# Kernel tuning notes

Hardware: AMD Instinct MI355X
Metric: run time of the kernel (lower is better)

Reference implementation:

```python
import jax, jax.numpy as jnp
import numpy as np

STRIDE = 1
PAD = 1

def setup_inputs() -> dict:
    key = jax.random.key(0)
    k1, k2 = jax.random.split(key)
    x = jax.random.normal(k1, (32, 128, 56, 56), dtype=jnp.float32)
    weight = jax.random.normal(k2, (256, 128, 3, 3), dtype=jnp.float32) * 0.1
    b = jnp.zeros((256,), dtype=jnp.float32)
    return {"x": x, "weight": weight, "b": b}

def reference(x, weight, b):
    # Binarize weights with sign (matches torch.sign: sign(0)=0), then plain conv2d.
    bw = jnp.sign(weight)
    out = jax.lax.conv_general_dilated(
        x, bw,
        window_strides=(STRIDE, STRIDE),
        padding=((PAD, PAD), (PAD, PAD)),
        dimension_numbers=("NCHW", "OIHW", "NCHW"),
    )
    return out + b[None, :, None, None]
```

## Files before the change

### kernel.cpp

```cpp
#include <hip/hip_runtime.h>
#include <hip/hip_bf16.h>

typedef __attribute__((ext_vector_type(8))) short bf16x8;
typedef __attribute__((ext_vector_type(4))) float f32x4;

#define CIN   128
#define COUT  256
#define NIMG  32
#define HWDIM 56
#define HPAD  58
#define KTOT  1152
#define HWIMG 3136
#define MTOT  100352
#define BN    256
#define BK    64
#define NT    18
#define BSZA  (COUT * BK)

__device__ __forceinline__ void gload16(const void* g, void* l) {
  __builtin_amdgcn_global_load_lds((const __attribute__((address_space(1))) void*)g,
                                   (__attribute__((address_space(3))) void*)l,
                                   16, 0, 0);
}

__global__ __launch_bounds__(256)
void prep_all(const float* __restrict__ x, const float* __restrict__ w,
              __hip_bfloat16* __restrict__ xp, __hip_bfloat16* __restrict__ wt) {
  __shared__ float tile[CIN * 57];
  const int bid = blockIdx.x;
  const int t = threadIdx.x;
  if (bid < NIMG * HPAD) {
    const int n = bid / HPAD;
    const int h = bid - n * HPAD;
    __hip_bfloat16* dstrow = xp + ((size_t)n * HPAD + h) * HPAD * CIN;
    int4 z; z.x = 0; z.y = 0; z.z = 0; z.w = 0;
    if (h == 0 || h == HPAD - 1) {
      for (int i = t; i < (HPAD * CIN) / 8; i += 256)
        reinterpret_cast<int4*>(dstrow)[i] = z;
      return;
    }
    const float* src = x + (size_t)n * CIN * HWIMG + (size_t)(h - 1) * HWDIM;
    for (int i = t; i < CIN * HWDIM; i += 256) {
      int c = i / HWDIM;
      int wd = i - c * HWDIM;
      tile[c * 57 + wd] = src[(size_t)c * HWIMG + wd];
    }
    if (t < 32) {
      int side = t >> 4;
      reinterpret_cast<int4*>(dstrow + (side ? (HPAD - 1) : 0) * CIN)[t & 15] = z;
    }
    __syncthreads();
    __hip_bfloat16* dst = dstrow + CIN;
    for (int o = t; o < HWDIM * 64; o += 256) {
      int wd = o >> 6;
      int c = (o & 63) * 2;
      __hip_bfloat162 pr;
      pr.x = __float2bfloat16(tile[c * 57 + wd]);
      pr.y = __float2bfloat16(tile[(c + 1) * 57 + wd]);
      *reinterpret_cast<__hip_bfloat162*>(dst + (size_t)wd * CIN + c) = pr;
    }
  } else {
    int o = (bid - NIMG * HPAD) * 256 + t;
    int cout = o / KTOT;
    int r = o - cout * KTOT;
    int tap = r >> 7;
    int cin = r & 127;
    float v = w[((size_t)cout * CIN + cin) * 9 + tap];
    wt[o] = __float2bfloat16(v > 0.f ? 1.f : (v < 0.f ? -1.f : 0.f));
  }
}

__global__ __launch_bounds__(512, 2)
void bconv(const short* __restrict__ xp, const short* __restrict__ wt,
           const float* __restrict__ bias, float* __restrict__ out) {
  __shared__ short lds[2][2 * BSZA];

  const int tid  = threadIdx.x;
  const int lane = tid & 63;
  const int wv   = tid >> 6;
  const int wm   = wv >> 2;
  const int wn   = wv & 3;
  const int s0   = blockIdx.x * BN;

  const int srow = tid >> 3;
  const int swz  = (tid & 7) ^ (srow & 7);

  int xb[2][2];
#pragma unroll
  for (int h = 0; h < 2; ++h)
#pragma unroll
    for (int r = 0; r < 2; ++r) {
      int m  = s0 + h * 128 + r * 64 + srow;
      int n  = m / HWIMG;
      int hw = m - n * HWIMG;
      int hh = hw / HWDIM;
      int ww = hw - hh * HWDIM;
      xb[h][r] = ((n * HPAD + hh) * HPAD + ww) * CIN + swz * 8;
    }
  const int wb = srow * KTOT + swz * 8;

#define STAGE_A(C, H, R, KO) \
  gload16(wt + ((H) * 128 + (R) * 64) * KTOT + wb + (KO), \
          &lds[C][(((H) * 128 + (R) * 64) + wv * 8) * BK])
#define STAGE_B(C, H, R, XKO) \
  gload16(xp + xb[H][R] + (XKO), \
          &lds[C][BSZA + (((H) * 128 + (R) * 64) + wv * 8) * BK])

  const int rlo = lane & 15;
  const int kq  = lane >> 4;
  const int swr = rlo & 7;

  f32x4 acc[8][4] = {};
  bf16x8 bx[4][2], af[2][2];

#define AF_LOAD(Q) \
  _Pragma("unroll") for (int f = 0; f < 2; ++f) \
  _Pragma("unroll") for (int kk = 0; kk < 2; ++kk) \
    af[f][kk] = *(const bf16x8*)&A[((Q) * 64 + wm * 32 + f * 16 + rlo) * BK + ((kk * 4 + kq) ^ swr) * 8];

#define MFMA_CLUSTER(Q) \
  __builtin_amdgcn_s_barrier(); \
  asm volatile("s_waitcnt lgkmcnt(0)" ::: "memory"); \
  __builtin_amdgcn_sched_barrier(0); \
  __builtin_amdgcn_s_setprio(1); \
  _Pragma("unroll") for (int f = 0; f < 2; ++f) \
  _Pragma("unroll") for (int nf = 0; nf < 4; ++nf) \
  _Pragma("unroll") for (int kk = 0; kk < 2; ++kk) \
    acc[2 * (Q) + f][nf] = __builtin_amdgcn_mfma_f32_16x16x32_bf16(af[f][kk], bx[nf][kk], acc[2 * (Q) + f][nf], 0, 0, 0); \
  __builtin_amdgcn_s_setprio(0);

  STAGE_B(0, 0, 0, 0); STAGE_B(0, 0, 1, 0);
  STAGE_B(0, 1, 0, 0); STAGE_B(0, 1, 1, 0);
  STAGE_A(0, 0, 0, 0); STAGE_A(0, 0, 1, 0);
  STAGE_A(0, 1, 0, 0); STAGE_A(0, 1, 1, 0);
  asm volatile("s_waitcnt vmcnt(0)" ::: "memory");
  __builtin_amdgcn_s_barrier();

  for (int t = 0; t < NT; ++t) {
    const int c  = t & 1;
    const int cn = c ^ 1;
    const short* A = &lds[c][0];
    const short* B = &lds[c][BSZA];
    const bool st = (t + 1 < NT);
    const int t1   = t + 1;
    const int tap1 = t1 >> 1;
    const int kh1  = tap1 / 3;
    const int kw1  = tap1 - kh1 * 3;
    const int xko1 = (kh1 * HPAD + kw1) * CIN + (t1 & 1) * BK;
    const int ko1  = t1 * BK;

#pragma unroll
    for (int nf = 0; nf < 4; ++nf)
#pragma unroll
      for (int kk = 0; kk < 2; ++kk)
        bx[nf][kk] = *(const bf16x8*)&B[(wn * 64 + nf * 16 + rlo) * BK + ((kk * 4 + kq) ^ swr) * 8];
    AF_LOAD(0)
    if (st) { STAGE_B(cn, 0, 0, xko1); STAGE_B(cn, 0, 1, xko1); }
    MFMA_CLUSTER(0)
    __builtin_amdgcn_s_barrier();

    AF_LOAD(1)
    if (st) { STAGE_B(cn, 1, 0, xko1); STAGE_B(cn, 1, 1, xko1); }
    MFMA_CLUSTER(1)
    if (st) asm volatile("s_waitcnt vmcnt(4)" ::: "memory");
    else    asm volatile("s_waitcnt vmcnt(0)" ::: "memory");
    __builtin_amdgcn_s_barrier();

    AF_LOAD(2)
    if (st) { STAGE_A(cn, 0, 0, ko1); STAGE_A(cn, 0, 1, ko1); }
    MFMA_CLUSTER(2)
    __builtin_amdgcn_s_barrier();

    AF_LOAD(3)
    if (st) { STAGE_A(cn, 1, 0, ko1); STAGE_A(cn, 1, 1, ko1); }
    MFMA_CLUSTER(3)
    if (st) asm volatile("s_waitcnt vmcnt(2)" ::: "memory");
    __builtin_amdgcn_s_barrier();
  }

  const int col = lane & 15;
  const int rg  = lane >> 4;
#pragma unroll
  for (int nf = 0; nf < 4; ++nf) {
    int m  = s0 + wn * 64 + nf * 16 + col;
    int n  = m / HWIMG;
    int hw = m - n * HWIMG;
    float* ob = out + (size_t)n * (COUT * HWIMG) + hw;
#pragma unroll
    for (int mi = 0; mi < 8; ++mi) {
      int c0 = (mi >> 1) * 64 + wm * 32 + (mi & 1) * 16 + rg * 4;
      const float4 bv = *reinterpret_cast<const float4*>(&bias[c0]);
      ob[(size_t)(c0 + 0) * HWIMG] = acc[mi][nf][0] + bv.x;
      ob[(size_t)(c0 + 1) * HWIMG] = acc[mi][nf][1] + bv.y;
      ob[(size_t)(c0 + 2) * HWIMG] = acc[mi][nf][2] + bv.z;
      ob[(size_t)(c0 + 3) * HWIMG] = acc[mi][nf][3] + bv.w;
    }
  }
#undef STAGE_A
#undef STAGE_B
#undef AF_LOAD
#undef MFMA_CLUSTER
}

extern "C" void kernel_launch(void* const* d_in, const int* in_sizes, int n_in,
                              void* d_out, int out_size, void* d_ws, size_t ws_size,
                              hipStream_t stream) {
  const float* x = (const float*)d_in[0];
  const float* w = (const float*)d_in[1];
  const float* b = (const float*)d_in[2];
  float* out = (float*)d_out;

  const size_t xp_elems = (size_t)NIMG * HPAD * HPAD * CIN;
  __hip_bfloat16* xp = (__hip_bfloat16*)d_ws;
  __hip_bfloat16* wt = xp + xp_elems;

  prep_all<<<NIMG * HPAD + (COUT * KTOT) / 256, 256, 0, stream>>>(x, w, xp, wt);
  bconv<<<MTOT / BN, 512, 0, stream>>>((const short*)xp, (const short*)wt, b, out);
}
```

Measured before the change: 98.42 us.

## Swap MFMA operands for vectorized stores and re-pipeline LDS/global staging

Swaps the MFMA operand order so each lane's accumulator holds four consecutive spatial outputs for one channel, which lets the epilogue write float4 stores instead of scattered scalar stores. Restructures the k-loop into four phases that preload fragments for two M-tiles at a time with double-buffered registers. Global-to-LDS staging is redistributed across the phases with new vmcnt wait points. Relies on 16-position groups never crossing an image boundary (3136 is divisible by 16), and adds register pressure from the extra fragment buffers.

New measurement: 98.57 us. Within noise of the previous version (+0.1%).

```diff
diff --git a/kernel.cpp b/kernel.cpp
--- a/kernel.cpp
+++ b/kernel.cpp
@@ -85,56 +85,51 @@
   const int srow = tid >> 3;
   const int swz  = (tid & 7) ^ (srow & 7);
 
-  int xb[2][2];
-#pragma unroll
-  for (int h = 0; h < 2; ++h)
-#pragma unroll
-    for (int r = 0; r < 2; ++r) {
-      int m  = s0 + h * 128 + r * 64 + srow;
-      int n  = m / HWIMG;
-      int hw = m - n * HWIMG;
-      int hh = hw / HWDIM;
-      int ww = hw - hh * HWDIM;
-      xb[h][r] = ((n * HPAD + hh) * HPAD + ww) * CIN + swz * 8;
-    }
+  int xb[4];
+#pragma unroll
+  for (int u = 0; u < 4; ++u) {
+    int m  = s0 + u * 64 + srow;
+    int n  = m / HWIMG;
+    int hw = m - n * HWIMG;
+    int hh = hw / HWDIM;
+    int ww = hw - hh * HWDIM;
+    xb[u] = ((n * HPAD + hh) * HPAD + ww) * CIN + swz * 8;
+  }
   const int wb = srow * KTOT + swz * 8;
 
-#define STAGE_A(C, H, R, KO) \
-  gload16(wt + ((H) * 128 + (R) * 64) * KTOT + wb + (KO), \
-          &lds[C][(((H) * 128 + (R) * 64) + wv * 8) * BK])
-#define STAGE_B(C, H, R, XKO) \
-  gload16(xp + xb[H][R] + (XKO), \
-          &lds[C][BSZA + (((H) * 128 + (R) * 64) + wv * 8) * BK])
+#define STAGE_A(C, U, KO) \
+  gload16(wt + ((U) * 64) * KTOT + wb + (KO), &lds[C][((U) * 64 + wv * 8) * BK])
+#define STAGE_B(C, U, XKO) \
+  gload16(xp + xb[U] + (XKO), &lds[C][BSZA + ((U) * 64 + wv * 8) * BK])
 
   const int rlo = lane & 15;
   const int kq  = lane >> 4;
   const int swr = rlo & 7;
 
   f32x4 acc[8][4] = {};
-  bf16x8 bx[4][2], af[2][2];
-
-#define AF_LOAD(Q) \
-  _Pragma("unroll") for (int f = 0; f < 2; ++f) \
+  bf16x8 bx[4][2], afA[2][2], afB[2][2];
+
+#define AF_LOAD(DST, MI) \
   _Pragma("unroll") for (int kk = 0; kk < 2; ++kk) \
-    af[f][kk] = *(const bf16x8*)&A[((Q) * 64 + wm * 32 + f * 16 + rlo) * BK + ((kk * 4 + kq) ^ swr) * 8];
-
-#define MFMA_CLUSTER(Q) \
-  __builtin_amdgcn_s_barrier(); \
-  asm volatile("s_waitcnt lgkmcnt(0)" ::: "memory"); \
-  __builtin_amdgcn_sched_barrier(0); \
-  __builtin_amdgcn_s_setprio(1); \
-  _Pragma("unroll") for (int f = 0; f < 2; ++f) \
-  _Pragma("unroll") for (int nf = 0; nf < 4; ++nf) \
-  _Pragma("unroll") for (int kk = 0; kk < 2; ++kk) \
-    acc[2 * (Q) + f][nf] = __builtin_amdgcn_mfma_f32_16x16x32_bf16(af[f][kk], bx[nf][kk], acc[2 * (Q) + f][nf], 0, 0, 0); \
-  __builtin_amdgcn_s_setprio(0);
-
-  STAGE_B(0, 0, 0, 0); STAGE_B(0, 0, 1, 0);
-  STAGE_B(0, 1, 0, 0); STAGE_B(0, 1, 1, 0);
-  STAGE_A(0, 0, 0, 0); STAGE_A(0, 0, 1, 0);
-  STAGE_A(0, 1, 0, 0); STAGE_A(0, 1, 1, 0);
-  asm volatile("s_waitcnt vmcnt(0)" ::: "memory");
-  __builtin_amdgcn_s_barrier();
+    DST[kk] = *(const bf16x8*)&A[((((MI) >> 1) * 64 + wm * 32 + ((MI) & 1) * 16 + rlo) * BK) + (((kk * 4) + kq) ^ swr) * 8];
+
+#define CLUSTER(MA, MB, AFR) \
+  _Pragma("unroll") for (int kk = 0; kk < 2; ++kk) { \
+    _Pragma("unroll") for (int nf = 0; nf < 4; ++nf) \
+      acc[MA][nf] = __builtin_amdgcn_mfma_f32_16x16x32_bf16(bx[nf][kk], AFR[0][kk], acc[MA][nf], 0, 0, 0); \
+    _Pragma("unroll") for (int nf = 0; nf < 4; ++nf) \
+      acc[MB][nf] = __builtin_amdgcn_mfma_f32_16x16x32_bf16(bx[nf][kk], AFR[1][kk], acc[MB][nf], 0, 0, 0); \
+  }
+
+#define BAR()  __builtin_amdgcn_s_barrier()
+#define SBAR() __builtin_amdgcn_sched_barrier(0)
+#define VM(N)  asm volatile("s_waitcnt vmcnt(" #N ")" ::: "memory")
+
+  STAGE_B(0, 0, 0); STAGE_B(0, 1, 0); STAGE_B(0, 2, 0); STAGE_B(0, 3, 0);
+  STAGE_A(0, 0, 0); STAGE_A(0, 1, 0);
+  STAGE_A(0, 2, 0); STAGE_A(0, 3, 0);
+  VM(2);
+  BAR();
 
   for (int t = 0; t < NT; ++t) {
     const int c  = t & 1;
@@ -153,53 +148,71 @@
     for (int nf = 0; nf < 4; ++nf)
 #pragma unroll
       for (int kk = 0; kk < 2; ++kk)
-        bx[nf][kk] = *(const bf16x8*)&B[(wn * 64 + nf * 16 + rlo) * BK + ((kk * 4 + kq) ^ swr) * 8];
-    AF_LOAD(0)
-    if (st) { STAGE_B(cn, 0, 0, xko1); STAGE_B(cn, 0, 1, xko1); }
-    MFMA_CLUSTER(0)
-    __builtin_amdgcn_s_barrier();
-
-    AF_LOAD(1)
-    if (st) { STAGE_B(cn, 1, 0, xko1); STAGE_B(cn, 1, 1, xko1); }
-    MFMA_CLUSTER(1)
-    if (st) asm volatile("s_waitcnt vmcnt(4)" ::: "memory");
-    else    asm volatile("s_waitcnt vmcnt(0)" ::: "memory");
-    __builtin_amdgcn_s_barrier();
-
-    AF_LOAD(2)
-    if (st) { STAGE_A(cn, 0, 0, ko1); STAGE_A(cn, 0, 1, ko1); }
-    MFMA_CLUSTER(2)
-    __builtin_amdgcn_s_barrier();
-
-    AF_LOAD(3)
-    if (st) { STAGE_A(cn, 1, 0, ko1); STAGE_A(cn, 1, 1, ko1); }
-    MFMA_CLUSTER(3)
-    if (st) asm volatile("s_waitcnt vmcnt(2)" ::: "memory");
-    __builtin_amdgcn_s_barrier();
+        bx[nf][kk] = *(const bf16x8*)&B[(wn * 64 + nf * 16 + rlo) * BK + (((kk * 4) + kq) ^ swr) * 8];
+    AF_LOAD(afA[0], 0) AF_LOAD(afA[1], 1) AF_LOAD(afB[0], 2) AF_LOAD(afB[1], 3)
+    if (st) { STAGE_B(cn, 0, xko1); STAGE_B(cn, 1, xko1); STAGE_B(cn, 2, xko1); }
+    BAR(); SBAR();
+    __builtin_amdgcn_s_setprio(1);
+    CLUSTER(0, 1, afA)
+    __builtin_amdgcn_s_setprio(0);
+    BAR();
+
+    if (st) { STAGE_B(cn, 3, xko1); STAGE_A(cn, 0, ko1); STAGE_A(cn, 1, ko1); }
+    BAR(); SBAR();
+    __builtin_amdgcn_s_setprio(1);
+    CLUSTER(2, 3, afB)
+    __builtin_amdgcn_s_setprio(0);
+    if (st) VM(6); else VM(0);
+    BAR();
+
+    AF_LOAD(afA[0], 4) AF_LOAD(afA[1], 5) AF_LOAD(afB[0], 6) AF_LOAD(afB[1], 7)
+    if (st) { STAGE_A(cn, 2, ko1); }
+    BAR(); SBAR();
+    __builtin_amdgcn_s_setprio(1);
+    CLUSTER(4, 5, afA)
+    __builtin_amdgcn_s_setprio(0);
+    BAR();
+
+    if (st) { STAGE_A(cn, 3, ko1); }
+    BAR(); SBAR();
+    __builtin_amdgcn_s_setprio(1);
+    CLUSTER(6, 7, afB)
+    __builtin_amdgcn_s_setprio(0);
+    if (st) VM(2);
+    BAR();
   }
 
   const int col = lane & 15;
   const int rg  = lane >> 4;
+  int nb[4], hwb[4];
 #pragma unroll
   for (int nf = 0; nf < 4; ++nf) {
-    int m  = s0 + wn * 64 + nf * 16 + col;
-    int n  = m / HWIMG;
-    int hw = m - n * HWIMG;
-    float* ob = out + (size_t)n * (COUT * HWIMG) + hw;
-#pragma unroll
-    for (int mi = 0; mi < 8; ++mi) {
-      int c0 = (mi >> 1) * 64 + wm * 32 + (mi & 1) * 16 + rg * 4;
-      const float4 bv = *reinterpret_cast<const float4*>(&bias[c0]);
-      ob[(size_t)(c0 + 0) * HWIMG] = acc[mi][nf][0] + bv.x;
-      ob[(size_t)(c0 + 1) * HWIMG] = acc[mi][nf][1] + bv.y;
-      ob[(size_t)(c0 + 2) * HWIMG] = acc[mi][nf][2] + bv.z;
-      ob[(size_t)(c0 + 3) * HWIMG] = acc[mi][nf][3] + bv.w;
+    int m16 = s0 + wn * 64 + nf * 16;
+    int n = m16 / HWIMG;
+    nb[nf]  = n;
+    hwb[nf] = m16 - n * HWIMG + rg * 4;
+  }
+#pragma unroll
+  for (int mi = 0; mi < 8; ++mi) {
+    int cc = (mi >> 1) * 64 + wm * 32 + (mi & 1) * 16 + col;
+    float bv = bias[cc];
+#pragma unroll
+    for (int nf = 0; nf < 4; ++nf) {
+      float4 v;
+      v.x = acc[mi][nf][0] + bv;
+      v.y = acc[mi][nf][1] + bv;
+      v.z = acc[mi][nf][2] + bv;
+      v.w = acc[mi][nf][3] + bv;
+      *reinterpret_cast<float4*>(out + ((size_t)nb[nf] * COUT + cc) * HWIMG + hwb[nf]) = v;
     }
   }
 #undef STAGE_A
 #undef STAGE_B
 #undef AF_LOAD
-#undef MFMA_CLUSTER
+#undef CLUSTER
+#undef BAR
+#undef SBAR
+#undef VM
 }
 
 extern "C" void kernel_launch(void* const* d_in, const int* in_sizes, int n_in,
```
